# Optimization experiments

Measured on AMD Instinct MI355X. Metric: run time of the kernel, lower is better.

## Reference

```python
import jax, jax.numpy as jnp
import numpy as np

EPS = 1e-5
NEG_SLOPE = 0.2
NUM_ITER = 3
C = 32            # channel
LCAPS = 40        # latent_caps_size
LVEC = 40         # latent_vec_size
PCAPS = 1287      # prim_caps_size (937 + 234 + 116)


def conv1d(x, w, stride, pad):
    # x: [B, Cin, L], w: [Cout, Cin, K]
    return jax.lax.conv_general_dilated(
        x, w, window_strides=(stride,), padding=[(pad, pad)],
        dimension_numbers=('NCH', 'OIH', 'NCH'))


def bn_lrelu(x, g, b, m, v):
    # eval-mode BatchNorm1d + LeakyReLU(0.2); x: [B, C, L]
    scale = (g * jax.lax.rsqrt(v + EPS))[None, :, None]
    y = (x - m[None, :, None]) * scale + b[None, :, None]
    return jnp.where(y >= 0, y, NEG_SLOPE * y)


def squash(t):
    sn = jnp.sum(t * t, axis=-1, keepdims=True)
    return sn * t / ((1.0 + sn) * jnp.sqrt(sn))


def setup_inputs() -> dict:
    key = jax.random.key(0)
    ks = jax.random.split(key, 10)
    data = jax.random.normal(ks[0], (32, 1, 4681), jnp.float32)
    conv1_w = 0.1 * jax.random.normal(ks[1], (C, 1, 5), jnp.float32)
    conv2_w = 0.1 * jax.random.normal(ks[2], (C, C, 5), jnp.float32)
    conv3_w = 0.1 * jax.random.normal(ks[3], (C, C, 4), jnp.float32)
    lin_w = 0.1 * jax.random.normal(ks[4], (C, C, 1), jnp.float32)
    bn_gamma = 1.0 + 0.1 * jax.random.normal(ks[5], (4, C), jnp.float32)
    bn_beta = 0.1 * jax.random.normal(ks[6], (4, C), jnp.float32)
    bn_mean = 0.1 * jax.random.normal(ks[7], (4, C), jnp.float32)
    bn_var = 0.5 + jax.random.uniform(ks[8], (4, C), jnp.float32)
    W_caps = 0.01 * jax.random.normal(ks[9], (LCAPS, PCAPS, LVEC, C), jnp.float32)
    return dict(data=data, conv1_w=conv1_w, conv2_w=conv2_w, conv3_w=conv3_w,
                lin_w=lin_w, bn_gamma=bn_gamma, bn_beta=bn_beta,
                bn_mean=bn_mean, bn_var=bn_var, W_caps=W_caps)


def reference(data, conv1_w, conv2_w, conv3_w, lin_w,
              bn_gamma, bn_beta, bn_mean, bn_var, W_caps):
    # OctreeKeyConv (eval mode: BN uses running stats, dropout off)
    x1 = bn_lrelu(conv1d(data, conv1_w, 5, 2), bn_gamma[0], bn_beta[0], bn_mean[0], bn_var[0])  # [B,32,937]
    x2 = bn_lrelu(conv1d(x1, conv2_w, 4, 0), bn_gamma[1], bn_beta[1], bn_mean[1], bn_var[1])    # [B,32,234]
    x3 = bn_lrelu(conv1d(x2, conv3_w, 2, 0), bn_gamma[2], bn_beta[2], bn_mean[2], bn_var[2])    # [B,32,116]
    x = jnp.concatenate([x1, x2, x3], axis=2)                                                    # [B,32,1287]
    x = bn_lrelu(conv1d(x, lin_w, 1, 0), bn_gamma[3], bn_beta[3], bn_mean[3], bn_var[3])
    x = jnp.transpose(x, (0, 2, 1))  # [B, 1287, 32]

    # LatentCapsLayer: u_hat[b,l,p,v] = sum_s W[l,p,v,s] x[b,p,s]
    u_hat = jnp.einsum('lpvs,bps->blpv', W_caps, x)  # [B,40,1287,40]
    u_det = jax.lax.stop_gradient(u_hat)
    B = x.shape[0]
    b_ij = jnp.zeros((B, LCAPS, PCAPS), x.dtype)
    v = None
    for it in range(NUM_ITER):
        c = jax.nn.softmax(b_ij, axis=1)  # softmax over latent caps
        if it == NUM_ITER - 1:
            v = squash(jnp.sum(c[..., None] * u_hat, axis=2, keepdims=True))  # [B,40,1,40]
        else:
            v = squash(jnp.sum(c[..., None] * u_det, axis=2, keepdims=True))
            b_ij = b_ij + jnp.sum(v * u_det, axis=-1)
    latent = jnp.squeeze(v, axis=2)       # [B,40,40]
    return jnp.sum(latent, axis=-1)       # [B,40]
```

## Files before the change

kernel.cpp:

```cpp
#include <hip/hip_runtime.h>

#define EPSB 1e-5f
#define NEG 0.2f

__device__ __forceinline__ float lrelu(float y) { return y >= 0.f ? y : NEG * y; }

typedef const __attribute__((address_space(1))) unsigned int gas1_u32;
typedef __attribute__((address_space(3))) unsigned int as3_u32;
__device__ __forceinline__ void gload16nt(const float* g, float* l) {
  __builtin_amdgcn_global_load_lds((gas1_u32*)g, (as3_u32*)l, 16, 0, 2);
}
#define WAITVM(N) asm volatile("s_waitcnt vmcnt(" #N ")" ::: "memory")

typedef float floatx4 __attribute__((ext_vector_type(4)));
typedef short bf16x8 __attribute__((ext_vector_type(8)));
__device__ __forceinline__ void nt_store4(float4 v, float* addr) {
  floatx4 w = {v.x, v.y, v.z, v.w};
  __builtin_nontemporal_store(w, (floatx4*)addr);
}

__device__ __forceinline__ unsigned short bfr(float f) {
  unsigned int b = __float_as_uint(f);
  return (unsigned short)((b + 0x7FFFu + ((b >> 16) & 1u)) >> 16);
}
__device__ __forceinline__ ushort4 f4bf(floatx4 a) {
  ushort4 r;
  r.x = bfr(a.x); r.y = bfr(a.y); r.z = bfr(a.z); r.w = bfr(a.w);
  return r;
}
__device__ __forceinline__ float4 bf4f(ushort4 h) {
  return make_float4(__uint_as_float((unsigned int)h.x << 16),
                     __uint_as_float((unsigned int)h.y << 16),
                     __uint_as_float((unsigned int)h.z << 16),
                     __uint_as_float((unsigned int)h.w << 16));
}

__device__ __forceinline__ void barrier_nodrain() {
  asm volatile("s_waitcnt lgkmcnt(0)" ::: "memory");
  __builtin_amdgcn_s_barrier();
  __builtin_amdgcn_sched_barrier(0);
}

__global__ __launch_bounds__(256) void k_front(
    const float* __restrict__ data, const float* __restrict__ w1,
    const float* __restrict__ w2, const float* __restrict__ w3,
    const float* __restrict__ lw, const float* __restrict__ bg,
    const float* __restrict__ bb, const float* __restrict__ bm,
    const float* __restrict__ bv, float* __restrict__ xt)
{
  __shared__ float x1s[32][132];
  __shared__ float x2s[32][40];
  __shared__ float x3s[32][20];
  const int b = blockIdx.x >> 3, q = blockIdx.x & 7, t = threadIdx.x;
  const int o1s = (937*q)/8, o1e = (937*(q+1))/8;
  const int o2s = (234*q)/8, o2e = (234*(q+1))/8;
  const int o3s = (116*q)/8, o3e = (116*(q+1))/8;
  int n2s = min(o2s, 2*o3s);
  int n2e = max(o2e, 2*(o3e-1)+4); if (n2e > 234) n2e = 234;
  int n1s = min(o1s, 4*n2s);
  int n1e = max(o1e, 4*(n2e-1)+5); if (n1e > 937) n1e = 937;
  const int w1w = n1e - n1s, w2w = n2e - n2s, w3w = o3e - o3s;

  for (int idx = t; idx < 32*w1w; idx += 256) {
    int c = idx / w1w, j = n1s + idx % w1w;
    float acc = 0.f;
    int base = 5*j - 2;
    #pragma unroll
    for (int k = 0; k < 5; ++k) {
      int pos = base + k;
      float d = (pos >= 0 && pos < 4681) ? data[b*4681 + pos] : 0.f;
      acc += w1[c*5 + k] * d;
    }
    float sc = bg[c] * rsqrtf(bv[c] + EPSB);
    x1s[c][j - n1s] = lrelu((acc - bm[c]) * sc + bb[c]);
  }
  __syncthreads();
  for (int idx = t; idx < 32*w2w; idx += 256) {
    int c = idx / w2w, j = n2s + idx % w2w;
    float acc = 0.f;
    int col = 4*j - n1s;
    for (int ci = 0; ci < 32; ++ci) {
      #pragma unroll
      for (int k = 0; k < 5; ++k) acc += w2[(c*32 + ci)*5 + k] * x1s[ci][col + k];
    }
    float sc = bg[32+c] * rsqrtf(bv[32+c] + EPSB);
    x2s[c][j - n2s] = lrelu((acc - bm[32+c]) * sc + bb[32+c]);
  }
  __syncthreads();
  for (int idx = t; idx < 32*w3w; idx += 256) {
    int c = idx / w3w, j = o3s + idx % w3w;
    float acc = 0.f;
    int col = 2*j - n2s;
    for (int ci = 0; ci < 32; ++ci) {
      #pragma unroll
      for (int k = 0; k < 4; ++k) acc += w3[(c*32 + ci)*4 + k] * x2s[ci][col + k];
    }
    float sc = bg[64+c] * rsqrtf(bv[64+c] + EPSB);
    x3s[c][j - o3s] = lrelu((acc - bm[64+c]) * sc + bb[64+c]);
  }
  __syncthreads();
  const int np1 = o1e - o1s, np2 = o2e - o2s, np3 = o3e - o3s;
  const int np = np1 + np2 + np3;
  for (int idx = t; idx < np*32; idx += 256) {
    int pi = idx >> 5, s = idx & 31;
    float acc = 0.f;
    int p;
    if (pi < np1) {
      int j = o1s + pi; p = j;
      int col = j - n1s;
      for (int ci = 0; ci < 32; ++ci) acc += lw[s*32 + ci] * x1s[ci][col];
    } else if (pi < np1 + np2) {
      int j = o2s + (pi - np1); p = 937 + j;
      int col = j - n2s;
      for (int ci = 0; ci < 32; ++ci) acc += lw[s*32 + ci] * x2s[ci][col];
    } else {
      int j = o3s + (pi - np1 - np2); p = 1171 + j;
      int col = j - o3s;
      for (int ci = 0; ci < 32; ++ci) acc += lw[s*32 + ci] * x3s[ci][col];
    }
    float sc = bg[96+s] * rsqrtf(bv[96+s] + EPSB);
    xt[p*1024 + b*32 + s] = lrelu((acc - bm[96+s]) * sc + bb[96+s]);
  }
}

__global__ __launch_bounds__(256) void k_uhat(
    const float* __restrict__ W, const float* __restrict__ xt,
    unsigned short* __restrict__ ubf, float* __restrict__ s0part)
{
  extern __shared__ float lds[];
  float* wbuf = lds;
  unsigned short* xs_hi = (unsigned short*)(lds + 10240);
  unsigned short* xs_lo = xs_hi + 10240;
  const int t = threadIdx.x;
  const int wv = t >> 6, lane = t & 63;
  const int wi = blockIdx.x*4 + wv;
  const int l = wi % 40, chunk = wi / 40;
  const int p0 = chunk * 8;
  float* myw = wbuf + wv * 2560;
  const float* Wl = W + (size_t)l * 1287 * 1280;
  const int row = lane & 15, g = lane >> 4;

  for (int idx = t; idx < 2048; idx += 256) {
    int pl = idx >> 8, rem = idx & 255;
    int b = rem >> 3, s4 = rem & 7;
    int pg = p0 + pl;
    float4 v = make_float4(0.f, 0.f, 0.f, 0.f);
    if (pg < 1287) v = *(const float4*)(xt + pg*1024 + b*32 + s4*4);
    unsigned int b0 = __float_as_uint(v.x), b1 = __float_as_uint(v.y);
    unsigned int b2 = __float_as_uint(v.z), b3 = __float_as_uint(v.w);
    ushort4 h, lo;
    h.x = (unsigned short)(b0 >> 16); h.y = (unsigned short)(b1 >> 16);
    h.z = (unsigned short)(b2 >> 16); h.w = (unsigned short)(b3 >> 16);
    lo.x = (unsigned short)(__float_as_uint(v.x - __uint_as_float(b0 & 0xffff0000u)) >> 16);
    lo.y = (unsigned short)(__float_as_uint(v.y - __uint_as_float(b1 & 0xffff0000u)) >> 16);
    lo.z = (unsigned short)(__float_as_uint(v.z - __uint_as_float(b2 & 0xffff0000u)) >> 16);
    lo.w = (unsigned short)(__float_as_uint(v.w - __uint_as_float(b3 & 0xffff0000u)) >> 16);
    int off = pl*1280 + b*40 + s4*4;
    *(ushort4*)(xs_hi + off) = h;
    *(ushort4*)(xs_lo + off) = lo;
  }
  #pragma unroll
  for (int i = 0; i < 5; ++i) {
    int gg = i*64 + lane, v = gg >> 3, s4 = (gg & 7) ^ (v & 7);
    gload16nt(Wl + (size_t)p0*1280 + (v*8 + s4)*4, myw + i*256);
  }
  #pragma unroll
  for (int i = 0; i < 5; ++i) {
    int gg = i*64 + lane, v = gg >> 3, s4 = (gg & 7) ^ (v & 7);
    gload16nt(Wl + (size_t)(p0+1)*1280 + (v*8 + s4)*4, myw + 1280 + i*256);
  }
  __syncthreads();

  floatx4 s0acc[2][3];
  #pragma unroll
  for (int mt = 0; mt < 2; ++mt)
    #pragma unroll
    for (int nt = 0; nt < 3; ++nt)
      s0acc[mt][nt] = (floatx4){0.f, 0.f, 0.f, 0.f};

  #pragma unroll
  for (int pp = 0; pp < 8; ++pp) {
    const int p = p0 + pp;
    if (p >= 1287) break;
    if (pp == 1)      WAITVM(11);
    else if (pp >= 2 && pp <= 6) WAITVM(17);
    else if (pp == 7) WAITVM(12);
    const float* wb = myw + (pp & 1)*1280;
    const unsigned short* xh = xs_hi + pp*1280;
    const unsigned short* xl = xs_lo + pp*1280;
    bf16x8 aH[2], aL[2];
    aH[0] = *(const bf16x8*)(xh + row*40 + g*8);
    aH[1] = *(const bf16x8*)(xh + (16 + row)*40 + g*8);
    aL[0] = *(const bf16x8*)(xl + row*40 + g*8);
    aL[1] = *(const bf16x8*)(xl + (16 + row)*40 + g*8);
    floatx4 acc[2][3];
    #pragma unroll
    for (int mt = 0; mt < 2; ++mt)
      #pragma unroll
      for (int nt = 0; nt < 3; ++nt)
        acc[mt][nt] = (floatx4){0.f, 0.f, 0.f, 0.f};
    #pragma unroll
    for (int nt = 0; nt < 3; ++nt) {
      int vq = nt*16 + row;
      bool valid = vq < 40;
      int vv = valid ? vq : 0;
      float4 w0 = *(const float4*)(wb + vv*32 + (((2*g) ^ (vv & 7)) << 2));
      float4 w1 = *(const float4*)(wb + vv*32 + (((2*g + 1) ^ (vv & 7)) << 2));
      float ws[8] = {w0.x, w0.y, w0.z, w0.w, w1.x, w1.y, w1.z, w1.w};
      bf16x8 bH, bL;
      #pragma unroll
      for (int j = 0; j < 8; ++j) {
        unsigned int bits = __float_as_uint(ws[j]);
        unsigned short hs = (unsigned short)(bits >> 16);
        float lf = ws[j] - __uint_as_float(bits & 0xffff0000u);
        unsigned short lsv = (unsigned short)(__float_as_uint(lf) >> 16);
        bH[j] = valid ? (short)hs : (short)0;
        bL[j] = valid ? (short)lsv : (short)0;
      }
      #pragma unroll
      for (int mt = 0; mt < 2; ++mt) {
        acc[mt][nt] = __builtin_amdgcn_mfma_f32_16x16x32_bf16(aH[mt], bH, acc[mt][nt], 0, 0, 0);
        acc[mt][nt] = __builtin_amdgcn_mfma_f32_16x16x32_bf16(aH[mt], bL, acc[mt][nt], 0, 0, 0);
        acc[mt][nt] = __builtin_amdgcn_mfma_f32_16x16x32_bf16(aL[mt], bH, acc[mt][nt], 0, 0, 0);
      }
    }
    if (pp < 6) {
      int psrc = p + 2; if (psrc > 1286) psrc = 1286;
      asm volatile("s_waitcnt lgkmcnt(0)" ::: "memory");
      __builtin_amdgcn_sched_barrier(0);
      #pragma unroll
      for (int i = 0; i < 5; ++i) {
        int gg = i*64 + lane, v = gg >> 3, s4 = (gg & 7) ^ (v & 7);
        gload16nt(Wl + (size_t)psrc*1280 + (v*8 + s4)*4, myw + (pp & 1)*1280 + i*256);
      }
    }
    #pragma unroll
    for (int mt = 0; mt < 2; ++mt)
      #pragma unroll
      for (int nt = 0; nt < 3; ++nt) {
        int vq = nt*16 + row;
        if (vq < 40) {
          int q4 = mt*4 + g;
          *(ushort4*)(ubf + ((size_t)(q4*1287 + p))*6400 + l*160 + vq*4) = f4bf(acc[mt][nt]);
          s0acc[mt][nt] += acc[mt][nt];
        }
      }
  }
  #pragma unroll
  for (int mt = 0; mt < 2; ++mt)
    #pragma unroll
    for (int nt = 0; nt < 3; ++nt) {
      int vq = nt*16 + row;
      if (vq < 40) {
        int q4 = mt*4 + g;
        *(floatx4*)(s0part + (size_t)chunk*51200 + l*1280 + vq*32 + q4*4) = s0acc[mt][nt];
      }
    }
}

__global__ __launch_bounds__(64) void k_squash0(
    const float* __restrict__ s0, float* __restrict__ v0t)
{
  const int b = blockIdx.x / 40, l = blockIdx.x % 40, t = threadIdx.x;
  float s = 0.f;
  if (t < 40) s = s0[(l*40 + t)*32 + b] * (1.f/40.f);
  float sq = s*s;
  #pragma unroll
  for (int d = 1; d < 64; d <<= 1) sq += __shfl_xor(sq, d);
  float scale = sq > 0.f ? sq / ((1.f + sq) * sqrtf(sq)) : 0.f;
  if (t < 40) v0t[((size_t)(b >> 2)*1600 + l*40 + t)*4 + (b & 3)] = s * scale;
}

__global__ __launch_bounds__(64) void k_squash1(
    const float* __restrict__ sred, const float* __restrict__ v0t,
    float* __restrict__ v1t, float* __restrict__ vsum)
{
  const int b = blockIdx.x / 40, l = blockIdx.x % 40, t = threadIdx.x;
  float s = 0.f;
  size_t off = ((size_t)(b >> 2)*1600 + l*40 + t)*4 + (b & 3);
  if (t < 40) s = sred[off];
  float sq = s*s;
  #pragma unroll
  for (int d = 1; d < 64; d <<= 1) sq += __shfl_xor(sq, d);
  float scale = sq > 0.f ? sq / ((1.f + sq) * sqrtf(sq)) : 0.f;
  if (t < 40) {
    float v1 = s * scale;
    v1t[off] = v1;
    vsum[off] = v0t[off] + v1;
  }
}

__global__ __launch_bounds__(64) void k_final(
    const float* __restrict__ sred, float* __restrict__ out)
{
  const int b = blockIdx.x / 40, l = blockIdx.x % 40, t = threadIdx.x;
  float s = 0.f;
  if (t < 40) s = sred[((size_t)(b >> 2)*1600 + l*40 + t)*4 + (b & 3)];
  float sq = s*s, ss = s;
  #pragma unroll
  for (int d = 1; d < 64; d <<= 1) { sq += __shfl_xor(sq, d); ss += __shfl_xor(ss, d); }
  float scale = sq > 0.f ? sq / ((1.f + sq) * sqrtf(sq)) : 0.f;
  if (t == 0) out[b*40 + l] = ss * scale;
}

#define RPC 9
#define NCHUNK 143
__global__ __launch_bounds__(400) void k_route8(
    const unsigned short* __restrict__ ubf, const float* __restrict__ vprev,
    float* __restrict__ spart, int rev)
{
  __shared__ float4 dred[2][400];
  __shared__ float dot_lds[160];
  __shared__ float c_lds[2][160];
  const int q4 = blockIdx.x & 7;
  const int chunk0 = blockIdx.x >> 3;
  const int chunk = rev ? (NCHUNK - 1 - chunk0) : chunk0;
  const int t = threadIdx.x;
  const int l = t / 10;
  const int p0 = chunk * RPC;
  const ushort4* u4 = (const ushort4*)ubf;
  const float4* vp4 = (const float4*)vprev + (size_t)q4*1600;

  float4 vv[4], s4[4], fu[2][4];
  ushort4 uu[3][4];
  #pragma unroll
  for (int j = 0; j < 4; ++j) {
    vv[j] = vp4[t*4 + j];
    s4[j] = make_float4(0.f, 0.f, 0.f, 0.f);
  }
  {
    const ushort4* up0 = u4 + ((size_t)q4*1287 + p0)*1600;
    const ushort4* up1 = u4 + ((size_t)q4*1287 + p0 + 1)*1600;
    #pragma unroll
    for (int j = 0; j < 4; ++j) { uu[0][j] = up0[t*4 + j]; uu[1][j] = up1[t*4 + j]; }
    #pragma unroll
    for (int j = 0; j < 4; ++j) fu[0][j] = bf4f(uu[0][j]);
    float4 dp = make_float4(0.f, 0.f, 0.f, 0.f);
    #pragma unroll
    for (int j = 0; j < 4; ++j) {
      dp.x += fu[0][j].x*vv[j].x; dp.y += fu[0][j].y*vv[j].y;
      dp.z += fu[0][j].z*vv[j].z; dp.w += fu[0][j].w*vv[j].w;
    }
    dred[0][t] = dp;
  }
  barrier_nodrain();

  #pragma unroll
  for (int pl = 0; pl < RPC; ++pl) {
    const size_t qp = (size_t)q4*1287 + p0 + pl;
    if (t < 160) {
      const int lr = t >> 2, b4 = t & 3;
      float d = 0.f;
      #pragma unroll
      for (int vq = 0; vq < 10; ++vq)
        d += ((const float*)&dred[pl & 1][lr*10 + vq])[b4];
      dot_lds[b4*40 + lr] = d;
    }
    if (pl >= 1) {
      const float* cl = c_lds[(pl - 1) & 1];
      float c0 = cl[l], c1 = cl[40 + l], c2 = cl[80 + l], c3 = cl[120 + l];
      #pragma unroll
      for (int j = 0; j < 4; ++j) {
        s4[j].x += fu[(pl - 1) & 1][j].x*c0; s4[j].y += fu[(pl - 1) & 1][j].y*c1;
        s4[j].z += fu[(pl - 1) & 1][j].z*c2; s4[j].w += fu[(pl - 1) & 1][j].w*c3;
      }
    }
    if (pl + 2 < RPC) {
      const ushort4* upn = u4 + (qp + 2)*1600;
      #pragma unroll
      for (int j = 0; j < 4; ++j) uu[(pl + 2) % 3][j] = upn[t*4 + j];
    }
    barrier_nodrain();
    if (t < 256) {
      const int b4 = t >> 6, ll = t & 63;
      float d = (ll < 40) ? dot_lds[b4*40 + ll] : -1e30f;
      float m = d;
      #pragma unroll
      for (int off = 32; off; off >>= 1) m = fmaxf(m, __shfl_xor(m, off));
      float e = expf(d - m);
      float Z = e;
      #pragma unroll
      for (int off = 32; off; off >>= 1) Z += __shfl_xor(Z, off);
      if (ll < 40) c_lds[pl & 1][b4*40 + ll] = e * (1.f / Z);
    }
    if (pl + 1 < RPC) {
      #pragma unroll
      for (int j = 0; j < 4; ++j) fu[(pl + 1) & 1][j] = bf4f(uu[(pl + 1) % 3][j]);
      float4 dp = make_float4(0.f, 0.f, 0.f, 0.f);
      #pragma unroll
      for (int j = 0; j < 4; ++j) {
        dp.x += fu[(pl + 1) & 1][j].x*vv[j].x; dp.y += fu[(pl + 1) & 1][j].y*vv[j].y;
        dp.z += fu[(pl + 1) & 1][j].z*vv[j].z; dp.w += fu[(pl + 1) & 1][j].w*vv[j].w;
      }
      dred[(pl + 1) & 1][t] = dp;
    }
    barrier_nodrain();
  }
  {
    const float* cl = c_lds[(RPC - 1) & 1];
    float c0 = cl[l], c1 = cl[40 + l], c2 = cl[80 + l], c3 = cl[120 + l];
    #pragma unroll
    for (int j = 0; j < 4; ++j) {
      s4[j].x += fu[(RPC - 1) & 1][j].x*c0; s4[j].y += fu[(RPC - 1) & 1][j].y*c1;
      s4[j].z += fu[(RPC - 1) & 1][j].z*c2; s4[j].w += fu[(RPC - 1) & 1][j].w*c3;
    }
  }
  float* sp = spart + ((size_t)chunk*8 + q4)*6400;
  #pragma unroll
  for (int j = 0; j < 4; ++j)
    nt_store4(s4[j], sp + (t*4 + j)*4);
}

__global__ __launch_bounds__(256) void k_reduceN(
    const float* __restrict__ src, float* __restrict__ sout, int n)
{
  const int w = blockIdx.x*256 + threadIdx.x;
  float s = 0.f;
  #pragma unroll 4
  for (int c = 0; c < n; ++c)
    s += __builtin_nontemporal_load(src + (size_t)c*51200 + w);
  sout[w] = s;
}

extern "C" void kernel_launch(void* const* d_in, const int* in_sizes, int n_in,
                              void* d_out, int out_size, void* d_ws, size_t ws_size,
                              hipStream_t stream)
{
  const float* data = (const float*)d_in[0];
  const float* w1   = (const float*)d_in[1];
  const float* w2   = (const float*)d_in[2];
  const float* w3   = (const float*)d_in[3];
  const float* lw   = (const float*)d_in[4];
  const float* bg   = (const float*)d_in[5];
  const float* bb   = (const float*)d_in[6];
  const float* bm   = (const float*)d_in[7];
  const float* bv   = (const float*)d_in[8];
  const float* W    = (const float*)d_in[9];
  float* out = (float*)d_out;

  unsigned short* ubf = (unsigned short*)d_ws;
  float* s0     = (float*)d_ws + 32947200;
  float* v0t    = s0 + 51200;
  float* v1t    = v0t + 51200;
  float* s1     = v1t + 51200;
  float* vsum   = s1 + 51200;
  float* xt     = vsum + 51200;
  float* big    = xt + 1317888;
  float* s0part = big;
  float* spart  = big;

  const int KU_LDS = 10240*4 + 2*10240*2;
  hipFuncSetAttribute((const void*)k_uhat,
                      hipFuncAttributeMaxDynamicSharedMemorySize, KU_LDS);

  k_front<<<256, 256, 0, stream>>>(data, w1, w2, w3, lw, bg, bb, bm, bv, xt);
  k_uhat<<<1610, 256, KU_LDS, stream>>>(W, xt, ubf, s0part);
  k_reduceN<<<200, 256, 0, stream>>>(s0part, s0, 161);
  k_squash0<<<1280, 64, 0, stream>>>(s0, v0t);

  k_route8<<<NCHUNK*8, 400, 0, stream>>>(ubf, v0t, spart, 1);
  k_reduceN<<<200, 256, 0, stream>>>(spart, s1, NCHUNK);
  k_squash1<<<1280, 64, 0, stream>>>(s1, v0t, v1t, vsum);

  k_route8<<<NCHUNK*8, 400, 0, stream>>>(ubf, vsum, spart, 0);
  k_reduceN<<<200, 256, 0, stream>>>(spart, s0, NCHUNK);
  k_final<<<1280, 64, 0, stream>>>(s0, out);
}
```

Before: 312.0 us.

## Stream W_caps directly into registers instead of async LDS staging

The k_uhat kernel no longer stages W rows into LDS through global_load_lds with hand-placed vmcnt waits. Each lane now loads its own W fragments with nontemporal vector loads into a two-deep register double buffer, prefetching the next p row while the current one is computed. This frees 40 KB of LDS per block, which may allow higher occupancy, and removes the LDS round trip and swizzle. The cost is more VGPRs, only one row of prefetch distance instead of two, and uncoalesced 16-byte strided global loads per lane.

```diff
diff --git a/kernel.cpp b/kernel.cpp
--- a/kernel.cpp
+++ b/kernel.cpp
@@ -4,19 +4,15 @@
 #define NEG 0.2f
 
 __device__ __forceinline__ float lrelu(float y) { return y >= 0.f ? y : NEG * y; }
-
-typedef const __attribute__((address_space(1))) unsigned int gas1_u32;
-typedef __attribute__((address_space(3))) unsigned int as3_u32;
-__device__ __forceinline__ void gload16nt(const float* g, float* l) {
-  __builtin_amdgcn_global_load_lds((gas1_u32*)g, (as3_u32*)l, 16, 0, 2);
-}
-#define WAITVM(N) asm volatile("s_waitcnt vmcnt(" #N ")" ::: "memory")
 
 typedef float floatx4 __attribute__((ext_vector_type(4)));
 typedef short bf16x8 __attribute__((ext_vector_type(8)));
 __device__ __forceinline__ void nt_store4(float4 v, float* addr) {
   floatx4 w = {v.x, v.y, v.z, v.w};
   __builtin_nontemporal_store(w, (floatx4*)addr);
+}
+__device__ __forceinline__ floatx4 nt_load4(const float* addr) {
+  return __builtin_nontemporal_load((const floatx4*)addr);
 }
 
 __device__ __forceinline__ unsigned short bfr(float f) {
@@ -128,17 +124,17 @@
     unsigned short* __restrict__ ubf, float* __restrict__ s0part)
 {
   extern __shared__ float lds[];
-  float* wbuf = lds;
-  unsigned short* xs_hi = (unsigned short*)(lds + 10240);
+  unsigned short* xs_hi = (unsigned short*)lds;
   unsigned short* xs_lo = xs_hi + 10240;
   const int t = threadIdx.x;
   const int wv = t >> 6, lane = t & 63;
   const int wi = blockIdx.x*4 + wv;
   const int l = wi % 40, chunk = wi / 40;
   const int p0 = chunk * 8;
-  float* myw = wbuf + wv * 2560;
   const float* Wl = W + (size_t)l * 1287 * 1280;
   const int row = lane & 15, g = lane >> 4;
+  const int vq0 = row, vq1 = 16 + row;
+  const int vq2 = (32 + row < 40) ? (32 + row) : 0;
 
   for (int idx = t; idx < 2048; idx += 256) {
     int pl = idx >> 8, rem = idx & 255;
@@ -159,17 +155,18 @@
     *(ushort4*)(xs_hi + off) = h;
     *(ushort4*)(xs_lo + off) = lo;
   }
-  #pragma unroll
-  for (int i = 0; i < 5; ++i) {
-    int gg = i*64 + lane, v = gg >> 3, s4 = (gg & 7) ^ (v & 7);
-    gload16nt(Wl + (size_t)p0*1280 + (v*8 + s4)*4, myw + i*256);
-  }
-  #pragma unroll
-  for (int i = 0; i < 5; ++i) {
-    int gg = i*64 + lane, v = gg >> 3, s4 = (gg & 7) ^ (v & 7);
-    gload16nt(Wl + (size_t)(p0+1)*1280 + (v*8 + s4)*4, myw + 1280 + i*256);
-  }
   __syncthreads();
+
+  floatx4 wr[2][6];
+  {
+    const float* base = Wl + (size_t)p0*1280;
+    wr[0][0] = nt_load4(base + vq0*32 + g*8);
+    wr[0][1] = nt_load4(base + vq0*32 + g*8 + 4);
+    wr[0][2] = nt_load4(base + vq1*32 + g*8);
+    wr[0][3] = nt_load4(base + vq1*32 + g*8 + 4);
+    wr[0][4] = nt_load4(base + vq2*32 + g*8);
+    wr[0][5] = nt_load4(base + vq2*32 + g*8 + 4);
+  }
 
   floatx4 s0acc[2][3];
   #pragma unroll
@@ -182,10 +179,17 @@
   for (int pp = 0; pp < 8; ++pp) {
     const int p = p0 + pp;
     if (p >= 1287) break;
-    if (pp == 1)      WAITVM(11);
-    else if (pp >= 2 && pp <= 6) WAITVM(17);
-    else if (pp == 7) WAITVM(12);
-    const float* wb = myw + (pp & 1)*1280;
+    const int cur = pp & 1, nxt = cur ^ 1;
+    {
+      int pn = p + 1; if (pn > 1286) pn = 1286;
+      const float* base = Wl + (size_t)pn*1280;
+      wr[nxt][0] = nt_load4(base + vq0*32 + g*8);
+      wr[nxt][1] = nt_load4(base + vq0*32 + g*8 + 4);
+      wr[nxt][2] = nt_load4(base + vq1*32 + g*8);
+      wr[nxt][3] = nt_load4(base + vq1*32 + g*8 + 4);
+      wr[nxt][4] = nt_load4(base + vq2*32 + g*8);
+      wr[nxt][5] = nt_load4(base + vq2*32 + g*8 + 4);
+    }
     const unsigned short* xh = xs_hi + pp*1280;
     const unsigned short* xl = xs_lo + pp*1280;
     bf16x8 aH[2], aL[2];
@@ -201,12 +205,10 @@
         acc[mt][nt] = (floatx4){0.f, 0.f, 0.f, 0.f};
     #pragma unroll
     for (int nt = 0; nt < 3; ++nt) {
-      int vq = nt*16 + row;
-      bool valid = vq < 40;
-      int vv = valid ? vq : 0;
-      float4 w0 = *(const float4*)(wb + vv*32 + (((2*g) ^ (vv & 7)) << 2));
-      float4 w1 = *(const float4*)(wb + vv*32 + (((2*g + 1) ^ (vv & 7)) << 2));
-      float ws[8] = {w0.x, w0.y, w0.z, w0.w, w1.x, w1.y, w1.z, w1.w};
+      const bool valid = (nt < 2) || (32 + row < 40);
+      float ws[8];
+      #pragma unroll
+      for (int j = 0; j < 4; ++j) { ws[j] = wr[cur][nt*2][j]; ws[4+j] = wr[cur][nt*2+1][j]; }
       bf16x8 bH, bL;
       #pragma unroll
       for (int j = 0; j < 8; ++j) {
@@ -222,16 +224,6 @@
         acc[mt][nt] = __builtin_amdgcn_mfma_f32_16x16x32_bf16(aH[mt], bH, acc[mt][nt], 0, 0, 0);
         acc[mt][nt] = __builtin_amdgcn_mfma_f32_16x16x32_bf16(aH[mt], bL, acc[mt][nt], 0, 0, 0);
         acc[mt][nt] = __builtin_amdgcn_mfma_f32_16x16x32_bf16(aL[mt], bH, acc[mt][nt], 0, 0, 0);
-      }
-    }
-    if (pp < 6) {
-      int psrc = p + 2; if (psrc > 1286) psrc = 1286;
-      asm volatile("s_waitcnt lgkmcnt(0)" ::: "memory");
-      __builtin_amdgcn_sched_barrier(0);
-      #pragma unroll
-      for (int i = 0; i < 5; ++i) {
-        int gg = i*64 + lane, v = gg >> 3, s4 = (gg & 7) ^ (v & 7);
-        gload16nt(Wl + (size_t)psrc*1280 + (v*8 + s4)*4, myw + (pp & 1)*1280 + i*256);
       }
     }
     #pragma unroll
@@ -449,7 +441,7 @@
   float* s0part = big;
   float* spart  = big;
 
-  const int KU_LDS = 10240*4 + 2*10240*2;
+  const int KU_LDS = 2*10240*2;
   hipFuncSetAttribute((const void*)k_uhat,
                       hipFuncAttributeMaxDynamicSharedMemorySize, KU_LDS);
 
```

Result: slower. 319.7 us (+2.5%).
